# Performance work log

Measured on AMD Instinct MI355X. Metric: run time of the kernel, lower is better.

The kernel has to match this reference:

```python
import jax, jax.numpy as jnp
import numpy as np

MARGIN = 0.1
LAMBDA_EFFECT = 0.5

B, T_V, K, T_S = 32, 8192, 64, 128


def setup_inputs() -> dict:
    key = jax.random.key(0)
    k1, k2, k3, k4, k5 = jax.random.split(key, 5)
    pred_orig = jax.random.normal(k1, (B, T_V), dtype=jnp.float32)
    pred_intervened = jax.random.normal(k2, (K, B, T_V), dtype=jnp.float32)
    intervened_indices = jax.random.randint(k3, (K,), 0, T_S, dtype=jnp.int32)
    # GT alignment mask: sparse-ish binary alignment between frames and sentences
    gt_mask = jax.random.bernoulli(k4, 0.2, (B, T_V, T_S)).astype(jnp.int32)
    # prefix-valid video mask: valid length per batch in [T_V//2, T_V]
    lengths = jax.random.randint(k5, (B,), T_V // 2, T_V + 1, dtype=jnp.int32)
    mask_video = (jnp.arange(T_V, dtype=jnp.int32)[None, :] < lengths[:, None]).astype(jnp.int32)
    return {
        "pred_orig": pred_orig,
        "pred_intervened": pred_intervened,
        "intervened_indices": intervened_indices,
        "gt_mask": gt_mask,
        "mask_video": mask_video,
    }


def reference(pred_orig, pred_intervened, intervened_indices, gt_mask, mask_video):
    # pred_orig: [B,T], pred_intervened: [K,B,T], gt_mask: [B,T,S], mask_video: [B,T]
    prob_orig = jax.nn.sigmoid(pred_orig)                 # [B,T]
    prob_int = jax.nn.sigmoid(pred_intervened)            # [K,B,T]
    effect = jnp.abs(prob_orig[None, :, :] - prob_int)    # [K,B,T]

    valid = mask_video.astype(bool)                       # [B,T] (prefix mask == :T_v_valid slice)
    # gather intervened sentence columns: [B,T,K] -> [K,B,T]
    gt_sel = jnp.transpose(gt_mask[:, :, intervened_indices], (2, 0, 1))

    aligned = (gt_sel > 0) & valid[None]                  # [K,B,T]
    non_aligned = (gt_sel == 0) & valid[None]             # [K,B,T]

    cnt_a = aligned.sum(axis=-1)                          # [K,B]
    cnt_n = non_aligned.sum(axis=-1)                      # [K,B]

    ea = jnp.sum(effect * aligned, axis=-1) / jnp.maximum(cnt_a, 1)
    en = jnp.sum(effect * non_aligned, axis=-1) / jnp.maximum(cnt_n, 1)

    per_pair = jnp.where((cnt_a > 0) & (cnt_n > 0),
                         jax.nn.relu(MARGIN - (ea - en)),
                         jnp.zeros_like(ea))
    num_interventions = pred_orig.shape[0] * pred_intervened.shape[0]
    alignment_consistency = per_pair.sum() / max(num_interventions, 1)
    total_intervention_loss = alignment_consistency * LAMBDA_EFFECT
    return alignment_consistency, total_intervention_loss
```

## Files before the change

kernel.cpp:

```cpp
#include <hip/hip_runtime.h>
#include <cstdint>

#define BB 32
#define TV 8192
#define KK 64
#define TS 128
#define MARGIN_F 0.1f
#define LAMBDA_F 0.5f

#define TT 128
static constexpr int KSTR = BB * TV;
static constexpr int NTILE = TV / TT;

__global__ __launch_bounds__(256, 4) void fused_kernel(
    const float* __restrict__ po, const float* __restrict__ pi,
    const int* __restrict__ idx, const int* __restrict__ gt,
    const int* __restrict__ mv,
    float* __restrict__ gsa, float* __restrict__ gsv,
    float* __restrict__ gca, int* __restrict__ len) {
  const int tid = threadIdx.x;
  const int lane = tid & 63;
  const int w = tid >> 6;

  const int bid = blockIdx.x;
  const int b = bid >> 6;
  const int tile = (bid & 63) ^ b;
  const int t0 = tile * TT;

  __shared__ unsigned long long ph[4][65];
  __shared__ unsigned sV[4];
  __shared__ float so[TT];

  const int rbase = b * TV + t0 + 32 * w;
  const int mvv = (lane < 32) ? mv[rbase + lane] : 0;
  const unsigned V32 = (unsigned)__ballot(mvv != 0);
  if (lane == 0) {
    sV[w] = V32;
    if (V32) atomicAdd(&len[b], __popc(V32));
  }
  if (tid < TT) so[tid] = __fdividef(1.f, 1.f + __expf(-po[b * TV + t0 + tid]));

  const int c = idx[lane];
  const int csel = c & 3, csh = c >> 2;
  const int h32 = (w & 1) * 32;
  unsigned long long plane = 0ull;
  if (V32 != 0u) {
    const int4* rowp = (const int4*)(gt + (size_t)rbase * TS);
#pragma unroll
    for (int batch = 0; batch < 2; ++batch) {
      int4 v[8];
#pragma unroll
      for (int i = 0; i < 8; ++i) v[i] = rowp[(batch * 8 + i) * 64 + lane];
#pragma unroll
      for (int i = 0; i < 8; ++i) {
        const int it = batch * 8 + i;
        const unsigned long long b0 = __ballot(v[i].x > 0);
        const unsigned long long b1 = __ballot(v[i].y > 0);
        const unsigned long long b2 = __ballot(v[i].z > 0);
        const unsigned long long b3 = __ballot(v[i].w > 0);
        const unsigned long long sel =
            (csel == 0) ? b0 : (csel == 1) ? b1 : (csel == 2) ? b2 : b3;
        plane |= ((sel >> csh) & 1ull) << (h32 + 2 * it);
        plane |= ((sel >> (32 + csh)) & 1ull) << (h32 + 2 * it + 1);
      }
    }
    plane &= ((unsigned long long)V32) << h32;
  }
  ph[w][lane] = plane;
  __syncthreads();

  if ((sV[0] | sV[1] | sV[2] | sV[3]) == 0u) return;

  const int bitpos = (lane & 31) * 2;
  const unsigned long long Vlo =
      (unsigned long long)sV[0] | ((unsigned long long)sV[1] << 32);
  const unsigned long long Vhi =
      (unsigned long long)sV[2] | ((unsigned long long)sV[3] << 32);
  const unsigned long long myV = (lane < 32) ? Vlo : Vhi;
  const unsigned vb2 = (unsigned)((myV >> bitpos) & 3ull);
  const float2 so2 = *(const float2*)&so[2 * lane];
  const float* pib = pi + (size_t)b * TV + t0 + 2 * lane;
  const int kbase = w * 16;

  float2 x[16];
#pragma unroll
  for (int i = 0; i < 16; ++i) {
    x[i] = make_float2(0.f, 0.f);
    if (vb2) x[i] = *(const float2*)(pib + (size_t)(kbase + i) * KSTR);
  }

  float sa[16], sv[16];
#pragma unroll
  for (int i = 0; i < 16; ++i) {
    const int k = kbase + i;
    const unsigned long long mine =
        (lane < 32) ? (ph[0][k] | ph[1][k]) : (ph[2][k] | ph[3][k]);
    const unsigned ab2 = (unsigned)((mine >> bitpos) & 3ull);
    const float e0 = fabsf(so2.x - __fdividef(1.f, 1.f + __expf(-x[i].x)));
    const float e1 = fabsf(so2.y - __fdividef(1.f, 1.f + __expf(-x[i].y)));
    float a = 0.f, vv = 0.f;
    if (vb2 & 1u) vv += e0;
    if (vb2 & 2u) vv += e1;
    if (ab2 & 1u) a += e0;
    if (ab2 & 2u) a += e1;
    sa[i] = a;
    sv[i] = vv;
  }

#pragma unroll
  for (int i = 0; i < 16; ++i) {
    float A = sa[i], Vv = sv[i];
#pragma unroll
    for (int off = 32; off; off >>= 1) {
      A += __shfl_xor(A, off);
      Vv += __shfl_xor(Vv, off);
    }
    if (lane == 0) {
      const int k = kbase + i;
      if (A != 0.f) atomicAdd(&gsa[k * BB + b], A);
      if (Vv != 0.f) atomicAdd(&gsv[k * BB + b], Vv);
      const int ca =
          __popcll(ph[0][k] | ph[1][k]) + __popcll(ph[2][k] | ph[3][k]);
      if (ca) atomicAdd(&gca[k * BB + b], (float)ca);
    }
  }
}

__global__ __launch_bounds__(256) void fin_kernel(
    const float* __restrict__ gsa, const float* __restrict__ gsv,
    const float* __restrict__ gca, const int* __restrict__ len,
    float* __restrict__ out) {
  float s = 0.f;
  for (int i = threadIdx.x; i < KK * BB; i += 256) {
    const int b = i & (BB - 1);
    const float ca = gca[i];
    const float cn = (float)len[b] - ca;
    if (ca > 0.f && cn > 0.f) {
      const float sa = gsa[i];
      const float sv = gsv[i];
      const float d = MARGIN_F - (sa / ca - (sv - sa) / cn);
      s += d > 0.f ? d : 0.f;
    }
  }
#pragma unroll
  for (int off = 32; off > 0; off >>= 1) s += __shfl_down(s, off);
  __shared__ float ws4[4];
  if ((threadIdx.x & 63) == 0) ws4[threadIdx.x >> 6] = s;
  __syncthreads();
  if (threadIdx.x == 0) {
    const float S = ws4[0] + ws4[1] + ws4[2] + ws4[3];
    const float ac = S * (1.0f / (float)(KK * BB));
    out[0] = ac;
    out[1] = ac * LAMBDA_F;
  }
}

extern "C" void kernel_launch(void* const* d_in, const int* in_sizes, int n_in,
                              void* d_out, int out_size, void* d_ws, size_t ws_size,
                              hipStream_t stream) {
  const float* pred_orig = (const float*)d_in[0];
  const float* pred_int  = (const float*)d_in[1];
  const int*   idx       = (const int*)d_in[2];
  const int*   gt        = (const int*)d_in[3];
  const int*   mv        = (const int*)d_in[4];
  float* out = (float*)d_out;

  float* gsa = (float*)d_ws;
  float* gsv = gsa + KK * BB;
  float* gca = gsv + KK * BB;
  int*   len = (int*)(gca + KK * BB);

  hipMemsetAsync(d_ws, 0, (size_t)(3 * KK * BB) * sizeof(float) + BB * sizeof(int),
                 stream);
  fused_kernel<<<BB * NTILE, 256, 0, stream>>>(
      pred_orig, pred_int, idx, gt, mv, gsa, gsv, gca, len);
  fin_kernel<<<1, 256, 0, stream>>>(gsa, gsv, gca, len, out);
}
```

Baseline: 303.0 us.

## Double tile width to 256 frames per block with float4 loads

```diff
diff --git a/kernel.cpp b/kernel.cpp
--- a/kernel.cpp
+++ b/kernel.cpp
@@ -8,7 +8,7 @@
 #define MARGIN_F 0.1f
 #define LAMBDA_F 0.5f
 
-#define TT 128
+#define TT 256
 static constexpr int KSTR = BB * TV;
 static constexpr int NTILE = TV / TT;
 
@@ -23,105 +23,113 @@
   const int w = tid >> 6;
 
   const int bid = blockIdx.x;
-  const int b = bid >> 6;
-  const int tile = (bid & 63) ^ b;
+  const int b = bid >> 5;
+  const int tile = ((bid & 31) + b) & 31;
   const int t0 = tile * TT;
 
-  __shared__ unsigned long long ph[4][65];
-  __shared__ unsigned sV[4];
+  __shared__ unsigned long long planes[4][65];
+  __shared__ unsigned long long sVg[4];
   __shared__ float so[TT];
 
-  const int rbase = b * TV + t0 + 32 * w;
-  const int mvv = (lane < 32) ? mv[rbase + lane] : 0;
-  const unsigned V32 = (unsigned)__ballot(mvv != 0);
+  const int r0 = b * TV + t0 + w * 64;
+  const unsigned long long V = __ballot(mv[r0 + lane] != 0);
   if (lane == 0) {
-    sV[w] = V32;
-    if (V32) atomicAdd(&len[b], __popc(V32));
+    sVg[w] = V;
+    if (V) atomicAdd(&len[b], __popcll(V));
   }
-  if (tid < TT) so[tid] = __fdividef(1.f, 1.f + __expf(-po[b * TV + t0 + tid]));
+  so[tid] = __fdividef(1.f, 1.f + __expf(-po[b * TV + t0 + tid]));
 
   const int c = idx[lane];
   const int csel = c & 3, csh = c >> 2;
-  const int h32 = (w & 1) * 32;
   unsigned long long plane = 0ull;
-  if (V32 != 0u) {
-    const int4* rowp = (const int4*)(gt + (size_t)rbase * TS);
+  if (V != 0ull) {
+    const int4* rowp = (const int4*)(gt + (size_t)r0 * TS);
 #pragma unroll
-    for (int batch = 0; batch < 2; ++batch) {
+    for (int batch = 0; batch < 4; ++batch) {
       int4 v[8];
 #pragma unroll
       for (int i = 0; i < 8; ++i) v[i] = rowp[(batch * 8 + i) * 64 + lane];
+      __builtin_amdgcn_sched_barrier(0);
 #pragma unroll
       for (int i = 0; i < 8; ++i) {
-        const int it = batch * 8 + i;
+        const int ch = batch * 8 + i;
         const unsigned long long b0 = __ballot(v[i].x > 0);
         const unsigned long long b1 = __ballot(v[i].y > 0);
         const unsigned long long b2 = __ballot(v[i].z > 0);
         const unsigned long long b3 = __ballot(v[i].w > 0);
         const unsigned long long sel =
             (csel == 0) ? b0 : (csel == 1) ? b1 : (csel == 2) ? b2 : b3;
-        plane |= ((sel >> csh) & 1ull) << (h32 + 2 * it);
-        plane |= ((sel >> (32 + csh)) & 1ull) << (h32 + 2 * it + 1);
+        plane |= ((sel >> csh) & 1ull) << (2 * ch);
+        plane |= ((sel >> (32 + csh)) & 1ull) << (2 * ch + 1);
       }
     }
-    plane &= ((unsigned long long)V32) << h32;
+    plane &= V;
   }
-  ph[w][lane] = plane;
+  planes[w][lane] = plane;
   __syncthreads();
 
-  if ((sV[0] | sV[1] | sV[2] | sV[3]) == 0u) return;
+  if ((sVg[0] | sVg[1] | sVg[2] | sVg[3]) == 0ull) return;
 
-  const int bitpos = (lane & 31) * 2;
-  const unsigned long long Vlo =
-      (unsigned long long)sV[0] | ((unsigned long long)sV[1] << 32);
-  const unsigned long long Vhi =
-      (unsigned long long)sV[2] | ((unsigned long long)sV[3] << 32);
-  const unsigned long long myV = (lane < 32) ? Vlo : Vhi;
-  const unsigned vb2 = (unsigned)((myV >> bitpos) & 3ull);
-  const float2 so2 = *(const float2*)&so[2 * lane];
-  const float* pib = pi + (size_t)b * TV + t0 + 2 * lane;
+  const int g = lane >> 4;
+  const int sh4 = (lane & 15) * 4;
+  const unsigned vb4 = (unsigned)((sVg[g] >> sh4) & 15ull);
+  const float4 so4 = *(const float4*)&so[lane * 4];
+  const float* pib = pi + (size_t)b * TV + t0 + lane * 4;
   const int kbase = w * 16;
 
-  float2 x[16];
+  float sa[16], sv[16];
+  int cn[16];
+
 #pragma unroll
-  for (int i = 0; i < 16; ++i) {
-    x[i] = make_float2(0.f, 0.f);
-    if (vb2) x[i] = *(const float2*)(pib + (size_t)(kbase + i) * KSTR);
-  }
-
-  float sa[16], sv[16];
+  for (int batch = 0; batch < 2; ++batch) {
+    float4 x[8];
 #pragma unroll
-  for (int i = 0; i < 16; ++i) {
-    const int k = kbase + i;
-    const unsigned long long mine =
-        (lane < 32) ? (ph[0][k] | ph[1][k]) : (ph[2][k] | ph[3][k]);
-    const unsigned ab2 = (unsigned)((mine >> bitpos) & 3ull);
-    const float e0 = fabsf(so2.x - __fdividef(1.f, 1.f + __expf(-x[i].x)));
-    const float e1 = fabsf(so2.y - __fdividef(1.f, 1.f + __expf(-x[i].y)));
-    float a = 0.f, vv = 0.f;
-    if (vb2 & 1u) vv += e0;
-    if (vb2 & 2u) vv += e1;
-    if (ab2 & 1u) a += e0;
-    if (ab2 & 2u) a += e1;
-    sa[i] = a;
-    sv[i] = vv;
+    for (int i = 0; i < 8; ++i) x[i] = make_float4(0.f, 0.f, 0.f, 0.f);
+    if (vb4) {
+#pragma unroll
+      for (int i = 0; i < 8; ++i)
+        x[i] = *(const float4*)(pib + (size_t)(kbase + batch * 8 + i) * KSTR);
+    }
+    __builtin_amdgcn_sched_barrier(0);
+#pragma unroll
+    for (int i = 0; i < 8; ++i) {
+      const int kk = batch * 8 + i;
+      const int k = kbase + kk;
+      const unsigned ab4 = (unsigned)((planes[g][k] >> sh4) & 15ull);
+      const float e0 = fabsf(so4.x - __fdividef(1.f, 1.f + __expf(-x[i].x)));
+      const float e1 = fabsf(so4.y - __fdividef(1.f, 1.f + __expf(-x[i].y)));
+      const float e2 = fabsf(so4.z - __fdividef(1.f, 1.f + __expf(-x[i].z)));
+      const float e3 = fabsf(so4.w - __fdividef(1.f, 1.f + __expf(-x[i].w)));
+      float a = 0.f, vv = 0.f;
+      if (ab4 & 1u) a += e0;
+      if (vb4 & 1u) vv += e0;
+      if (ab4 & 2u) a += e1;
+      if (vb4 & 2u) vv += e1;
+      if (ab4 & 4u) a += e2;
+      if (vb4 & 4u) vv += e2;
+      if (ab4 & 8u) a += e3;
+      if (vb4 & 8u) vv += e3;
+      sa[kk] = a;
+      sv[kk] = vv;
+      cn[kk] = __popc(ab4);
+    }
   }
 
 #pragma unroll
-  for (int i = 0; i < 16; ++i) {
-    float A = sa[i], Vv = sv[i];
+  for (int kk = 0; kk < 16; ++kk) {
+    float A = sa[kk], Vv = sv[kk];
+    int C = cn[kk];
 #pragma unroll
     for (int off = 32; off; off >>= 1) {
       A += __shfl_xor(A, off);
       Vv += __shfl_xor(Vv, off);
+      C += __shfl_xor(C, off);
     }
     if (lane == 0) {
-      const int k = kbase + i;
+      const int k = kbase + kk;
       if (A != 0.f) atomicAdd(&gsa[k * BB + b], A);
       if (Vv != 0.f) atomicAdd(&gsv[k * BB + b], Vv);
-      const int ca =
-          __popcll(ph[0][k] | ph[1][k]) + __popcll(ph[2][k] | ph[3][k]);
-      if (ca) atomicAdd(&gca[k * BB + b], (float)ca);
+      if (C) atomicAdd(&gca[k * BB + b], (float)C);
     }
   }
 }
```

After: 267.3 us. -11.8%, faster.
